# Kernel tuning notes

Hardware: AMD Instinct MI355X
Metric: run time of the kernel (lower is better)

Reference implementation:

```python
import jax, jax.numpy as jnp
import numpy as np

B, C, H, W = 2, 128, 64, 64
CR4 = C // 4  # hidden width of linear_weight / bias branches
SOFTMAX_SCALE = 1.0


def _leaky(z):
    return jnp.where(z >= 0, z, 0.2 * z)


def _conv1x1(x, w, b):
    # x: [B,Ci,H,W], w: [Co,Ci], b: [Co]
    return jnp.einsum('oc,bchw->bohw', w, x) + b[None, :, None, None]


def setup_inputs() -> dict:
    key = jax.random.key(0)
    ks = jax.random.split(key, 16)
    def n(k, shape, s=0.05):
        return jax.random.normal(k, shape, jnp.float32) * s
    return {
        'x': jax.random.normal(ks[0], (B, C, H, W), jnp.float32),
        'value_w': n(ks[1], (C, C)), 'value_b': n(ks[2], (C,)),
        'query_w': n(ks[3], (C, C)), 'query_b': n(ks[4], (C,)),
        'lw1_w': n(ks[5], (CR4, C)), 'lw1_b': n(ks[6], (CR4,)),
        'lw2_w': n(ks[7], (1, CR4)), 'lw2_b': n(ks[8], (1,)),
        'bi1_w': n(ks[9], (CR4, C)), 'bi1_b': n(ks[10], (CR4,)),
        'bi2_w': n(ks[11], (1, CR4)), 'bi2_b': n(ks[12], (1,)),
        'lin_w': n(ks[13], (C, C, 3, 3)), 'lin_b': n(ks[14], (C,)),
    }


def reference(x, value_w, value_b, query_w, query_b,
              lw1_w, lw1_b, lw2_w, lw2_b,
              bi1_w, bi1_b, bi2_w, bi2_b,
              lin_w, lin_b):
    # value / query 1x1 projections
    x1 = _conv1x1(x, value_w, value_b)   # [B,C,H,W]
    x2 = _conv1x1(x, query_w, query_b)   # [B,C,H,W]
    # dynamic per-pixel weight / bias maps (two 1x1 convs + LeakyReLU)
    wei = _conv1x1(_leaky(_conv1x1(x2, lw1_w, lw1_b)), lw2_w, lw2_b)  # [B,1,H,W]
    bii = _conv1x1(_leaky(_conv1x1(x2, bi1_w, bi1_b)), bi2_w, bi2_b)  # [B,1,H,W]

    Bn, Cn, Hn, Wn = x.shape
    L = Hn * Wn  # one 1x1 patch per spatial location (ksize=1, stride=1)
    # query patches [B,L,C]; normalize each patch to (at least 1e-4) unit norm
    wq = x2.transpose(0, 2, 3, 1).reshape(Bn, L, Cn)
    wnorm = wq / jnp.maximum(jnp.linalg.norm(wq, axis=2, keepdims=True), 1e-4)
    # attention scores: per-sample conv2d(xi, wi_normed) == batched matmul
    yi = jnp.einsum('bchw,blc->blhw', x2, wnorm)  # [B,L,H,W]
    # sparse gating
    sparse = jax.nn.relu(yi - yi.mean(axis=1, keepdims=True) * wei + bii)
    sr = (sparse != 0.0).astype(yi.dtype)
    yi = yi * sparse
    yi = jax.nn.softmax(yi * SOFTMAX_SCALE, axis=1)
    yi = jnp.maximum(yi * sr, 1e-8)
    # reconstruct with value patches (conv_transpose2d with 1x1 kernels)
    raw = x1.transpose(0, 2, 3, 1).reshape(Bn, L, Cn)
    out = jnp.einsum('blhw,blc->bchw', yi, raw)  # / (ksize*ksize) == /1
    # final 3x3 conv + LeakyReLU + residual
    y = jax.lax.conv_general_dilated(out, lin_w, (1, 1), 'SAME',
                                     dimension_numbers=('NCHW', 'OIHW', 'NCHW'))
    y = _leaky(y + lin_b[None, :, None, None])
    return y + x
```

## Files before the change

### kernel.cpp

```cpp
#include <hip/hip_runtime.h>
#include <hip/hip_bf16.h>
#include <math.h>

#define BB 2
#define C 128
#define L 4096
#define CR4 32
#define RS 4

typedef unsigned short ushort_t;
typedef __attribute__((ext_vector_type(8))) short s16x8;
typedef __attribute__((ext_vector_type(4))) float f32x4;

__device__ inline float leaky(float z) { return (z >= 0.f) ? z : 0.2f * z; }

__device__ inline unsigned short f2bf(float f) {
    unsigned int u = __builtin_bit_cast(unsigned int, f);
    unsigned int r = (u + 0x7fffu + ((u >> 16) & 1u)) >> 16;
    return (unsigned short)r;
}
__device__ inline float bf2f(unsigned short b) {
    unsigned int u = ((unsigned int)b) << 16;
    return __builtin_bit_cast(float, u);
}
__device__ inline unsigned int cvtpk(float lo, float hi) {
    unsigned int r;
    asm("v_cvt_pk_bf16_f32 %0, %1, %2" : "=v"(r) : "v"(lo), "v"(hi));
    return r;
}

__global__ __launch_bounds__(256) void k_wcomp(
    const float* __restrict__ vw, const float* __restrict__ vb,
    const float* __restrict__ qw, const float* __restrict__ qb,
    const float* __restrict__ lw1w, const float* __restrict__ lw1b,
    const float* __restrict__ bi1w, const float* __restrict__ bi1b,
    ushort_t* __restrict__ WQV, float* __restrict__ biasv)
{
    const int mt = blockIdx.x;
    const int t = threadIdx.x;
    const int kk = t >> 6, lane = t & 63;
    const int row = mt * 16 + (lane & 15);
    const int k0 = kk * 32 + (lane >> 4) * 8;
    s16x8 v;
    if (row < 128) {
        #pragma unroll
        for (int j = 0; j < 8; ++j) v[j] = (short)f2bf(vw[row * 128 + k0 + j]);
    } else if (row < 256) {
        #pragma unroll
        for (int j = 0; j < 8; ++j) v[j] = (short)f2bf(qw[(row - 128) * 128 + k0 + j]);
    } else {
        const float* w1 = (row < 288) ? lw1w + (row - 256) * 128
                                      : bi1w + (row - 288) * 128;
        float acc[8] = {0.f, 0.f, 0.f, 0.f, 0.f, 0.f, 0.f, 0.f};
        #pragma unroll 2
        for (int k = 0; k < 128; ++k) {
            float wv_ = w1[k];
            const float* qr = qw + k * 128 + k0;
            #pragma unroll
            for (int j = 0; j < 8; ++j) acc[j] = fmaf(wv_, qr[j], acc[j]);
        }
        #pragma unroll
        for (int j = 0; j < 8; ++j) v[j] = (short)f2bf(acc[j]);
    }
    *(s16x8*)(WQV + ((size_t)(mt * 4 + kk) * 64 + lane) * 8) = v;

    if (t < 16) {
        int rr = mt * 16 + t;
        float bv;
        if (rr < 128) bv = vb[rr];
        else if (rr < 256) bv = qb[rr - 128];
        else {
            const float* w1 = (rr < 288) ? lw1w + (rr - 256) * 128
                                         : bi1w + (rr - 288) * 128;
            float a = (rr < 288) ? lw1b[rr - 256] : bi1b[rr - 288];
            for (int k = 0; k < 128; ++k) a = fmaf(w1[k], qb[k], a);
            bv = a;
        }
        biasv[rr] = bv;
    }
}

__global__ __launch_bounds__(256, 1) void k_proj2(
    const float* __restrict__ x, const ushort_t* __restrict__ WQV,
    const float* __restrict__ biasv,
    const float* __restrict__ lw2w, const float* __restrict__ lw2b,
    const float* __restrict__ bi2w, const float* __restrict__ bi2b,
    ushort_t* __restrict__ x2a, ushort_t* __restrict__ x1g,
    float* __restrict__ weiA, float* __restrict__ biiA, float* __restrict__ scA,
    float* __restrict__ cpart)
{
    __shared__ __align__(16) char smem[16384 + 1536];
    char* xT = smem;
    float* biasLDS = (float*)(smem + 16384);
    float* w2LDS = biasLDS + 320;

    const int t = threadIdx.x;
    const int blk = blockIdx.x;
    const int part = blockIdx.y;
    const int b = blk >> 6;
    const int p0 = (blk & 63) * 64;
    const int wv = t >> 6, lane = t & 63, n = lane & 15, g = lane >> 4;

    biasLDS[t] = biasv[t];
    if (t < 64) {
        biasLDS[256 + t] = biasv[256 + t];
        w2LDS[t] = (t < 32) ? lw2w[t] : bi2w[t - 32];
    }

    const int pl = t & 63, cg = t >> 6;
    const float* xb = x + (size_t)b * C * L + p0 + pl;
    #pragma unroll
    for (int i = 0; i < 16; ++i) {
        int c = cg * 32 + i * 2;
        float v0 = xb[(size_t)c * L];
        float v1 = xb[(size_t)(c + 1) * L];
        int slot = c >> 3;
        int offs = (c * 2) & 15;
        int byte = pl * 256 + (((slot ^ (pl & 15)) << 4) | offs);
        *(unsigned int*)(xT + byte) = cvtpk(v0, v1);
    }
    __syncthreads();

    const int brow = wv * 16 + n;
    const int p = p0 + wv * 16 + n;
    const size_t bL = (size_t)b * L;

    if (part == 0) {
        const int mtm[12] = {0, 1, 2, 3, 4, 5, 6, 7, 16, 17, 18, 19};
        f32x4 acc[12];
        #pragma unroll
        for (int i = 0; i < 12; ++i) acc[i] = (f32x4){0.f, 0.f, 0.f, 0.f};
        #pragma unroll
        for (int kk = 0; kk < 4; ++kk) {
            const s16x8 bfr = *(const s16x8*)(xT + brow * 256 + (((4 * kk + g) ^ n) << 4));
            #pragma unroll
            for (int i = 0; i < 12; ++i) {
                const s16x8 afr = *(const s16x8*)(WQV + ((size_t)(mtm[i] * 4 + kk) * 64 + lane) * 8);
                acc[i] = __builtin_amdgcn_mfma_f32_16x16x32_bf16(afr, bfr, acc[i], 0, 0, 0);
            }
        }
        #pragma unroll
        for (int i = 0; i < 12; ++i) {
            const f32x4 bv = *(const f32x4*)(biasLDS + mtm[i] * 16 + g * 4);
            acc[i][0] += bv[0]; acc[i][1] += bv[1];
            acc[i][2] += bv[2]; acc[i][3] += bv[3];
        }
        #pragma unroll
        for (int i = 0; i < 8; ++i)
            #pragma unroll
            for (int r = 0; r < 4; ++r)
                x1g[((size_t)b * C + i * 16 + g * 4 + r) * L + p] = f2bf(acc[i][r]);
        float pw = 0.f, pbb = 0.f;
        #pragma unroll
        for (int i = 8; i < 10; ++i)
            #pragma unroll
            for (int r = 0; r < 4; ++r)
                pw = fmaf(w2LDS[(i - 8) * 16 + g * 4 + r], leaky(acc[i][r]), pw);
        #pragma unroll
        for (int i = 10; i < 12; ++i)
            #pragma unroll
            for (int r = 0; r < 4; ++r)
                pbb = fmaf(w2LDS[32 + (i - 10) * 16 + g * 4 + r], leaky(acc[i][r]), pbb);
        pw += __shfl_xor(pw, 16, 64);  pw += __shfl_xor(pw, 32, 64);
        pbb += __shfl_xor(pbb, 16, 64); pbb += __shfl_xor(pbb, 32, 64);
        if (g == 0) {
            weiA[bL + p] = pw + lw2b[0];
            biiA[bL + p] = pbb + bi2b[0];
        }
    } else {
        f32x4 acc[8];
        #pragma unroll
        for (int i = 0; i < 8; ++i) acc[i] = (f32x4){0.f, 0.f, 0.f, 0.f};
        #pragma unroll
        for (int kk = 0; kk < 4; ++kk) {
            const s16x8 bfr = *(const s16x8*)(xT + brow * 256 + (((4 * kk + g) ^ n) << 4));
            #pragma unroll
            for (int i = 0; i < 8; ++i) {
                const s16x8 afr = *(const s16x8*)(WQV + ((size_t)((8 + i) * 4 + kk) * 64 + lane) * 8);
                acc[i] = __builtin_amdgcn_mfma_f32_16x16x32_bf16(afr, bfr, acc[i], 0, 0, 0);
            }
        }
        #pragma unroll
        for (int i = 0; i < 8; ++i) {
            const f32x4 bv = *(const f32x4*)(biasLDS + (8 + i) * 16 + g * 4);
            acc[i][0] += bv[0]; acc[i][1] += bv[1];
            acc[i][2] += bv[2]; acc[i][3] += bv[3];
        }
        float pn = 0.f;
        #pragma unroll
        for (int i = 0; i < 8; ++i)
            #pragma unroll
            for (int r = 0; r < 4; ++r) pn = fmaf(acc[i][r], acc[i][r], pn);
        pn += __shfl_xor(pn, 16, 64);
        pn += __shfl_xor(pn, 32, 64);
        float scv = fmaxf(sqrtf(pn), 1e-4f);
        float dinv = 1.f / scv;
        if (g == 0) scA[bL + p] = scv;
        #pragma unroll
        for (int i = 0; i < 8; ++i) {
            uint2 uu;
            uu.x = cvtpk(acc[i][0] * dinv, acc[i][1] * dinv);
            uu.y = cvtpk(acc[i][2] * dinv, acc[i][3] * dinv);
            *(uint2*)(x2a + (bL + p) * C + i * 16 + g * 4) = uu;
        }
        float sv[32];
        #pragma unroll
        for (int i = 0; i < 8; ++i)
            #pragma unroll
            for (int r = 0; r < 4; ++r)
                sv[i * 4 + r] = acc[i][r] * dinv;
        #pragma unroll
        for (int mask = 1; mask <= 8; mask <<= 1)
            #pragma unroll
            for (int i = 0; i < 32; ++i)
                sv[i] += __shfl_xor(sv[i], mask, 64);
        __syncthreads();
        float* sumsh = (float*)xT;
        if (n == 0) {
            #pragma unroll
            for (int i = 0; i < 32; ++i) {
                int ch = (i >> 2) * 16 + g * 4 + (i & 3);
                sumsh[wv * 128 + ch] = sv[i];
            }
        }
        __syncthreads();
        if (t < 128)
            cpart[(size_t)blk * 128 + t] =
                (sumsh[t] + sumsh[128 + t]) + (sumsh[256 + t] + sumsh[384 + t]);
    }
}

__global__ __launch_bounds__(128) void k_cb(
    const float* __restrict__ cpart, float* __restrict__ cbv)
{
    const int b = blockIdx.x, t = threadIdx.x;
    float s = 0.f;
    #pragma unroll 4
    for (int j = 0; j < 64; ++j) s += cpart[(size_t)(b * 64 + j) * 128 + t];
    cbv[b * 128 + t] = s * (1.f / (float)L);
}

__global__ __launch_bounds__(256, 2) void k_attn(
    const ushort_t* __restrict__ x2a, const ushort_t* __restrict__ x1g,
    const float* __restrict__ scA, const float* __restrict__ weiA,
    const float* __restrict__ biiA, const float* __restrict__ cbv,
    ushort_t* __restrict__ Opb, float* __restrict__ Mp, float* __restrict__ Zp)
{
    __shared__ __align__(16) char smem[73728];

    const int t = threadIdx.x;
    const int w = t >> 6, lane = t & 63, n = lane & 15, g = lane >> 4;
    char* Pw = smem + 65536 + w * 2048;

    const int blk = blockIdx.x;
    const int q = blk & (RS - 1);
    const int colt = (blk >> 2) & 63;
    const int b = blk >> 8;
    const int p = colt * 64 + w * 16 + n;
    const size_t bL = (size_t)b * L;

    const s16x8* qrow = (const s16x8*)(x2a + (bL + p) * C);
    const float scp = scA[bL + p];
    s16x8 bq[4];
    float dot = 0.f;
    #pragma unroll
    for (int kk = 0; kk < 4; ++kk) {
        s16x8 raw = qrow[kk * 4 + g];
        const float* cbp = cbv + b * 128 + kk * 32 + g * 8;
        s16x8 u;
        #pragma unroll
        for (int j = 0; j < 8; ++j) {
            float rv = bf2f((unsigned short)raw[j]) * scp;
            u[j] = (short)f2bf(rv);
            dot = fmaf(cbp[j], rv, dot);
        }
        bq[kk] = u;
    }
    dot += __shfl_xor(dot, 16, 64);
    dot += __shfl_xor(dot, 32, 64);
    const float tq = fmaf(weiA[bL + p], dot, -biiA[bL + p]);

    f32x4 Oacc[8];
    #pragma unroll
    for (int ct = 0; ct < 8; ++ct) Oacc[ct] = (f32x4){0.f, 0.f, 0.f, 0.f};
    float Mrun = 0.f, Zrun = 0.f;

    const int l0base = q * (L / RS);
    const char* x2src = (const char*)(x2a + (bL + l0base) * C);
    const char* x1src = (const char*)(x1g + (size_t)b * C * L);

    #define STAGE_X2(buf, tile_)                                                         \
        {   const char* sb = x2src + (size_t)(tile_) * 64 * 256;                          \
            _Pragma("unroll")                                                             \
            for (int rr = 0; rr < 4; ++rr) {                                              \
                int slot = rr * 256 + t;                                                  \
                int lrow = slot >> 4, uu = slot & 15;                                     \
                const char* gp = sb + lrow * 256 + (((uu ^ (lrow & 7))) << 4);            \
                char* lp = (buf) + ((rr * 256 + w * 64) << 4);                            \
                __builtin_amdgcn_global_load_lds(                                         \
                    (const __attribute__((address_space(1))) unsigned int*)gp,            \
                    (__attribute__((address_space(3))) unsigned int*)lp, 16, 0, 0);       \
            } }
    #define STAGE_X1(buf, l0_)                                                            \
        {   _Pragma("unroll")                                                             \
            for (int rr = 0; rr < 4; ++rr) {                                              \
                int slot = rr * 256 + t;                                                  \
                int cr = slot >> 3, uu = slot & 7;                                        \
                const char* gp = x1src + ((size_t)cr * L + (l0_) + ((uu ^ (cr & 7)) << 3)) * 2; \
                char* lp = (buf) + ((rr * 256 + w * 64) << 4);                            \
                __builtin_amdgcn_global_load_lds(                                         \
                    (const __attribute__((address_space(1))) unsigned int*)gp,            \
                    (__attribute__((address_space(3))) unsigned int*)lp, 16, 0, 0);       \
            } }

    char* Abuf0 = smem;          char* Abuf1 = smem + 16384;
    char* Xbuf0 = smem + 32768;  char* Xbuf1 = smem + 49152;

    STAGE_X2(Abuf0, 0);
    STAGE_X1(Xbuf0, l0base);
    __syncthreads();

    const int swz = n & 7;
    const int NT = L / RS / 64;

    #pragma unroll 1
    for (int tile = 0; tile < NT; ++tile) {
        char* Ab = (tile & 1) ? Abuf1 : Abuf0;
        char* Xb = (tile & 1) ? Xbuf1 : Xbuf0;
        if (tile + 1 < NT) {
            char* An = (tile & 1) ? Abuf0 : Abuf1;
            char* Xn = (tile & 1) ? Xbuf0 : Xbuf1;
            STAGE_X2(An, tile + 1);
            STAGE_X1(Xn, l0base + (tile + 1) * 64);
        }

        f32x4 s4[4];
        #pragma unroll
        for (int lt = 0; lt < 4; ++lt) s4[lt] = (f32x4){0.f, 0.f, 0.f, 0.f};
        __builtin_amdgcn_s_setprio(1);
        #pragma unroll
        for (int kk = 0; kk < 4; ++kk) {
            #pragma unroll
            for (int lt = 0; lt < 4; ++lt) {
                const s16x8 a = *(const s16x8*)(Ab + (16 * lt + n) * 256 +
                                                (((4 * kk + g) ^ swz) << 4));
                s4[lt] = __builtin_amdgcn_mfma_f32_16x16x32_bf16(a, bq[kk], s4[lt], 0, 0, 0);
            }
        }
        __builtin_amdgcn_s_setprio(0);

        float vv[16], sps[16];
        #pragma unroll
        for (int lt = 0; lt < 4; ++lt) {
            #pragma unroll
            for (int r = 0; r < 4; ++r) {
                float s = s4[lt][r];
                float sp = s - tq;
                sps[lt * 4 + r] = sp;
                vv[lt * 4 + r] = s * fmaxf(sp, 0.f);
            }
        }
        float tm[8];
        #pragma unroll
        for (int i = 0; i < 8; ++i) tm[i] = fmaxf(vv[2 * i], vv[2 * i + 1]);
        #pragma unroll
        for (int i = 0; i < 4; ++i) tm[i] = fmaxf(tm[2 * i], tm[2 * i + 1]);
        float tmax = fmaxf(fmaxf(tm[0], tm[1]), fmaxf(tm[2], tm[3]));
        tmax = fmaxf(tmax, __shfl_xor(tmax, 16, 64));
        tmax = fmaxf(tmax, __shfl_xor(tmax, 32, 64));

        if (!__all(tmax <= Mrun + 8.f)) {
            float Mn = fmaxf(Mrun, tmax);
            float so = __expf(Mrun - Mn);
            Mrun = Mn;
            Zrun *= so;
            #pragma unroll
            for (int ct = 0; ct < 8; ++ct) {
                Oacc[ct][0] *= so; Oacc[ct][1] *= so;
                Oacc[ct][2] *= so; Oacc[ct][3] *= so;
            }
        }

        #pragma unroll
        for (int lt = 0; lt < 4; ++lt) {
            float e0 = __expf(vv[lt * 4 + 0] - Mrun);
            float e1 = __expf(vv[lt * 4 + 1] - Mrun);
            float e2 = __expf(vv[lt * 4 + 2] - Mrun);
            float e3 = __expf(vv[lt * 4 + 3] - Mrun);
            Zrun += (e0 + e1) + (e2 + e3);
            float p0 = sps[lt * 4 + 0] > 0.f ? e0 : 0.f;
            float p1 = sps[lt * 4 + 1] > 0.f ? e1 : 0.f;
            float p2 = sps[lt * 4 + 2] > 0.f ? e2 : 0.f;
            float p3 = sps[lt * 4 + 3] > 0.f ? e3 : 0.f;
            int ulog = 2 * lt + (g >> 1);
            int byte = n * 128 + ((ulog ^ swz) << 4) + ((g & 1) << 3);
            uint2 uu;
            uu.x = cvtpk(p0, p1);
            uu.y = cvtpk(p2, p3);
            *(uint2*)(Pw + byte) = uu;
        }

        __builtin_amdgcn_s_setprio(1);
        #pragma unroll
        for (int kk2 = 0; kk2 < 2; ++kk2) {
            const s16x8 pb = *(const s16x8*)(Pw + n * 128 + (((4 * kk2 + g) ^ swz) << 4));
            #pragma unroll
            for (int ct = 0; ct < 8; ++ct) {
                const s16x8 a = *(const s16x8*)(Xb + (16 * ct + n) * 128 +
                                                (((4 * kk2 + g) ^ swz) << 4));
                Oacc[ct] = __builtin_amdgcn_mfma_f32_16x16x32_bf16(a, pb, Oacc[ct], 0, 0, 0);
            }
        }
        __builtin_amdgcn_s_setprio(0);
        __syncthreads();
    }
    #undef STAGE_X2
    #undef STAGE_X1

    float z = Zrun;
    z += __shfl_xor(z, 16, 64);
    z += __shfl_xor(z, 32, 64);

    const size_t sset = (size_t)(q * BB + b);
    ushort_t* ob = Opb + (sset * L + p) * C;
    #pragma unroll
    for (int ct = 0; ct < 8; ++ct) {
        uint2 uu;
        uu.x = cvtpk(Oacc[ct][0], Oacc[ct][1]);
        uu.y = cvtpk(Oacc[ct][2], Oacc[ct][3]);
        *(uint2*)(ob + 16 * ct + 4 * g) = uu;
    }
    if (g == 0) {
        Mp[sset * L + p] = Mrun;
        Zp[sset * L + p] = z;
    }
}

__global__ __launch_bounds__(256) void k_merge(
    const ushort_t* __restrict__ Opb, const float* __restrict__ Mp,
    const float* __restrict__ Zp, ushort_t* __restrict__ attnb)
{
    const int idx = blockIdx.x * 256 + threadIdx.x;
    const int c4 = idx & 31;
    const int p = (idx >> 5) & 4095;
    const int b = idx >> 17;
    size_t is[RS];
    float M = -1e30f;
    float Mq[RS], Zq[RS];
    #pragma unroll
    for (int q = 0; q < RS; ++q) {
        is[q] = (size_t)(q * BB + b) * L + p;
        Mq[q] = Mp[is[q]];
        Zq[q] = Zp[is[q]];
        M = fmaxf(M, Mq[q]);
    }
    float Zt = 0.f;
    float aq[RS];
    #pragma unroll
    for (int q = 0; q < RS; ++q) {
        aq[q] = __expf(Mq[q] - M);
        Zt = fmaf(Zq[q], aq[q], Zt);
    }
    float zi = 1.f / Zt;
    float r0 = 0.f, r1 = 0.f, r2 = 0.f, r3 = 0.f;
    #pragma unroll
    for (int q = 0; q < RS; ++q) {
        float s = aq[q] * zi;
        const ushort4 o = *(const ushort4*)(Opb + is[q] * C + c4 * 4);
        r0 = fmaf(bf2f(o.x), s, r0);
        r1 = fmaf(bf2f(o.y), s, r1);
        r2 = fmaf(bf2f(o.z), s, r2);
        r3 = fmaf(bf2f(o.w), s, r3);
    }
    uint2 uu;
    uu.x = cvtpk(r0, r1);
    uu.y = cvtpk(r2, r3);
    *(uint2*)(attnb + ((size_t)b * L + p) * C + c4 * 4) = uu;
}

__global__ __launch_bounds__(256) void k_wrep(
    const float* __restrict__ lw, ushort_t* __restrict__ W3)
{
    const int tid = blockIdx.x * 256 + threadIdx.x;
    const int s = tid >> 9;
    const int r = tid & 511;
    const int mt = r >> 6, lane = r & 63;
    const int co = mt * 16 + (lane & 15), g = lane >> 4;
    const int kk = s >> 2, kc = s & 3;
    const int ci0 = kc * 32 + g * 8;
    s16x8 v;
    #pragma unroll
    for (int j = 0; j < 8; ++j)
        v[j] = (short)f2bf(lw[((size_t)co * 128 + ci0 + j) * 9 + kk]);
    *(s16x8*)(W3 + (size_t)tid * 8) = v;
}

__global__ __launch_bounds__(256, 1) void k_conv(
    const ushort_t* __restrict__ attnb, const float* __restrict__ x,
    const ushort_t* __restrict__ W3, const float* __restrict__ lb,
    float* __restrict__ out)
{
    __shared__ __align__(16) char smem[65536];
    char* attnT = smem;
    char* Wb0 = smem + 49152;
    char* Wb1 = smem + 57344;

    const int t = threadIdx.x;
    const int wv = t >> 6, lane = t & 63, n = lane & 15, g = lane >> 4;
    const int h = blockIdx.x;
    const int half = blockIdx.y;
    const int b = blockIdx.z;

    const char* asrc = (const char*)attnb + ((size_t)b * L + (size_t)(h - 1) * 64) * C * 2;
    #pragma unroll
    for (int rr = 0; rr < 3; ++rr) {
        if ((unsigned)(h - 1 + rr) < 64u) {
            #pragma unroll
            for (int qq = 0; qq < 4; ++qq) {
                int slot = rr * 1024 + qq * 256 + t;
                int lrow = slot >> 4, uu = slot & 15;
                const char* gp = asrc + lrow * 256 + ((uu ^ (lrow & 7)) << 4);
                char* lp = attnT + ((rr * 1024 + qq * 256 + wv * 64) << 4);
                __builtin_amdgcn_global_load_lds(
                    (const __attribute__((address_space(1))) unsigned int*)gp,
                    (__attribute__((address_space(3))) unsigned int*)lp, 16, 0, 0);
            }
        }
    }
    #define STAGE_W(buf, s_)                                                              \
        {   _Pragma("unroll")                                                             \
            for (int qq = 0; qq < 2; ++qq) {                                              \
                const char* gp = (const char*)W3 + ((size_t)(s_) * 512 + qq * 256 + t) * 16; \
                char* lp = (buf) + ((qq * 256 + wv * 64) << 4);                           \
                __builtin_amdgcn_global_load_lds(                                         \
                    (const __attribute__((address_space(1))) unsigned int*)gp,            \
                    (__attribute__((address_space(3))) unsigned int*)lp, 16, 0, 0);       \
            } }

    STAGE_W(Wb0, 0);
    __syncthreads();

    f32x4 acc[2][2];
    #pragma unroll
    for (int mi = 0; mi < 2; ++mi)
        #pragma unroll
        for (int nt = 0; nt < 2; ++nt) acc[mi][nt] = (f32x4){0.f, 0.f, 0.f, 0.f};

    const s16x8 zer = {0, 0, 0, 0, 0, 0, 0, 0};

    #pragma unroll 1
    for (int s = 0; s < 36; ++s) {
        char* Wc = (s & 1) ? Wb1 : Wb0;
        if (s + 1 < 36) {
            char* Wn = (s & 1) ? Wb0 : Wb1;
            STAGE_W(Wn, s + 1);
        }
        const int kk = s >> 2, kc = s & 3;
        const int kh = kk / 3, kw = kk - kh * 3;
        const int dh = kh - 1, dw = kw - 1;
        const bool hval = ((unsigned)(h + dh) < 64u);

        s16x8 af0 = *(const s16x8*)(Wc + (((2 * wv) * 64 + lane) << 4));
        s16x8 af1 = *(const s16x8*)(Wc + (((2 * wv + 1) * 64 + lane) << 4));

        #pragma unroll
        for (int nt = 0; nt < 2; ++nt) {
            int pl = half * 32 + nt * 16 + n;
            int wd = pl + dw;
            bool val = hval && ((unsigned)wd < 64u);
            int wc = wd < 0 ? 0 : (wd > 63 ? 63 : wd);
            int lrow = (dh + 1) * 64 + wc;
            s16x8 bf_ = *(const s16x8*)(attnT + lrow * 256 +
                                        (((kc * 4 + g) ^ (lrow & 7)) << 4));
            if (!val) bf_ = zer;
            acc[0][nt] = __builtin_amdgcn_mfma_f32_16x16x32_bf16(af0, bf_, acc[0][nt], 0, 0, 0);
            acc[1][nt] = __builtin_amdgcn_mfma_f32_16x16x32_bf16(af1, bf_, acc[1][nt], 0, 0, 0);
        }
        __syncthreads();
    }
    #undef STAGE_W

    const float* xb = x + (size_t)b * C * L + h * 64;
    float* ob = out + (size_t)b * C * L + h * 64;
    #pragma unroll
    for (int mi = 0; mi < 2; ++mi) {
        #pragma unroll
        for (int r = 0; r < 4; ++r) {
            int co = (2 * wv + mi) * 16 + g * 4 + r;
            float bias = lb[co];
            #pragma unroll
            for (int nt = 0; nt < 2; ++nt) {
                int p_ = half * 32 + nt * 16 + n;
                float v = leaky(acc[mi][nt][r] + bias);
                ob[(size_t)co * L + p_] = v + xb[(size_t)co * L + p_];
            }
        }
    }
}

extern "C" void kernel_launch(void* const* d_in, const int* in_sizes, int n_in,
                              void* d_out, int out_size, void* d_ws, size_t ws_size,
                              hipStream_t stream) {
    const float* x     = (const float*)d_in[0];
    const float* vw    = (const float*)d_in[1];
    const float* vb    = (const float*)d_in[2];
    const float* qw    = (const float*)d_in[3];
    const float* qb    = (const float*)d_in[4];
    const float* lw1w  = (const float*)d_in[5];
    const float* lw1b  = (const float*)d_in[6];
    const float* lw2w  = (const float*)d_in[7];
    const float* lw2b  = (const float*)d_in[8];
    const float* bi1w  = (const float*)d_in[9];
    const float* bi1b  = (const float*)d_in[10];
    const float* bi2w  = (const float*)d_in[11];
    const float* bi2b  = (const float*)d_in[12];
    const float* lw    = (const float*)d_in[13];
    const float* lb    = (const float*)d_in[14];
    float* out = (float*)d_out;

    char* ws = (char*)d_ws;
    ushort_t* x2a  = (ushort_t*)ws;
    ushort_t* x1g  = (ushort_t*)(ws + 2097152);
    ushort_t* Opb  = (ushort_t*)(ws + 4194304);
    ushort_t* WQV  = (ushort_t*)(ws + 4194304);
    float* biasv = (float*)(ws + 4194304 + 81920);
    float* weiA  = (float*)(ws + 12582912);
    float* biiA  = weiA + BB * L;
    float* scA   = biiA + BB * L;
    float* Mp    = scA + BB * L;
    float* Zp    = Mp + RS * BB * L;
    float* cpart = Zp + RS * BB * L;
    float* cbv   = cpart + 128 * 128;
    ushort_t* W3 = x1g;
    ushort_t* attnb = x2a;

    hipLaunchKernelGGL(k_wcomp, dim3(20), dim3(256), 0, stream,
                       vw, vb, qw, qb, lw1w, lw1b, bi1w, bi1b, WQV, biasv);

    hipLaunchKernelGGL(k_proj2, dim3(128, 2), dim3(256), 0, stream,
                       x, WQV, biasv, lw2w, lw2b, bi2w, bi2b,
                       x2a, x1g, weiA, biiA, scA, cpart);

    hipLaunchKernelGGL(k_cb, dim3(BB), dim3(128), 0, stream, cpart, cbv);

    hipLaunchKernelGGL(k_attn, dim3(BB * 64 * RS), dim3(256), 0, stream,
                       x2a, x1g, scA, weiA, biiA, cbv, Opb, Mp, Zp);

    hipLaunchKernelGGL(k_wrep, dim3(72), dim3(256), 0, stream, lw, W3);

    hipLaunchKernelGGL(k_merge, dim3(BB * L * C / 4 / 256), dim3(256), 0, stream,
                       Opb, Mp, Zp, attnb);

    hipLaunchKernelGGL(k_conv, dim3(64, 2, BB), dim3(256), 0, stream,
                       attnb, x, W3, lb, out);
}
```

Before: 105.4 us.

## Fold small kernels into neighbours and stream conv weights from global

The channel-mean reduction kernel is removed: each attention block now sums cpart itself into shared memory, with the query preparation moved after the first barrier. The merge and weight-repack kernels are combined into one launch that branches on block index. The 3x3 conv stops staging weights through LDS with a barrier per step and instead prefetches weight fragments straight from global into registers two steps ahead. Together these remove two launches and the per-step conv syncs, at the cost of redundant cpart reads in every attention block and global-latency exposure on the conv weight loads.

```diff
diff --git a/kernel.cpp b/kernel.cpp
--- a/kernel.cpp
+++ b/kernel.cpp
@@ -230,23 +230,14 @@
     }
 }
 
-__global__ __launch_bounds__(128) void k_cb(
-    const float* __restrict__ cpart, float* __restrict__ cbv)
-{
-    const int b = blockIdx.x, t = threadIdx.x;
-    float s = 0.f;
-    #pragma unroll 4
-    for (int j = 0; j < 64; ++j) s += cpart[(size_t)(b * 64 + j) * 128 + t];
-    cbv[b * 128 + t] = s * (1.f / (float)L);
-}
-
 __global__ __launch_bounds__(256, 2) void k_attn(
     const ushort_t* __restrict__ x2a, const ushort_t* __restrict__ x1g,
     const float* __restrict__ scA, const float* __restrict__ weiA,
-    const float* __restrict__ biiA, const float* __restrict__ cbv,
+    const float* __restrict__ biiA, const float* __restrict__ cpart,
     ushort_t* __restrict__ Opb, float* __restrict__ Mp, float* __restrict__ Zp)
 {
     __shared__ __align__(16) char smem[73728];
+    __shared__ float cbsh[128];
 
     const int t = threadIdx.x;
     const int w = t >> 6, lane = t & 63, n = lane & 15, g = lane >> 4;
@@ -259,31 +250,13 @@
     const int p = colt * 64 + w * 16 + n;
     const size_t bL = (size_t)b * L;
 
-    const s16x8* qrow = (const s16x8*)(x2a + (bL + p) * C);
-    const float scp = scA[bL + p];
-    s16x8 bq[4];
-    float dot = 0.f;
-    #pragma unroll
-    for (int kk = 0; kk < 4; ++kk) {
-        s16x8 raw = qrow[kk * 4 + g];
-        const float* cbp = cbv + b * 128 + kk * 32 + g * 8;
-        s16x8 u;
-        #pragma unroll
-        for (int j = 0; j < 8; ++j) {
-            float rv = bf2f((unsigned short)raw[j]) * scp;
-            u[j] = (short)f2bf(rv);
-            dot = fmaf(cbp[j], rv, dot);
-        }
-        bq[kk] = u;
-    }
-    dot += __shfl_xor(dot, 16, 64);
-    dot += __shfl_xor(dot, 32, 64);
-    const float tq = fmaf(weiA[bL + p], dot, -biiA[bL + p]);
-
-    f32x4 Oacc[8];
-    #pragma unroll
-    for (int ct = 0; ct < 8; ++ct) Oacc[ct] = (f32x4){0.f, 0.f, 0.f, 0.f};
-    float Mrun = 0.f, Zrun = 0.f;
+    if (t < 128) {
+        float s = 0.f;
+        const float* cp = cpart + (size_t)(b * 64) * 128 + t;
+        #pragma unroll 4
+        for (int j = 0; j < 64; ++j) s += cp[(size_t)j * 128];
+        cbsh[t] = s * (1.f / (float)L);
+    }
 
     const int l0base = q * (L / RS);
     const char* x2src = (const char*)(x2a + (bL + l0base) * C);
@@ -320,6 +293,32 @@
     STAGE_X1(Xbuf0, l0base);
     __syncthreads();
 
+    const s16x8* qrow = (const s16x8*)(x2a + (bL + p) * C);
+    const float scp = scA[bL + p];
+    s16x8 bq[4];
+    float dot = 0.f;
+    #pragma unroll
+    for (int kk = 0; kk < 4; ++kk) {
+        s16x8 raw = qrow[kk * 4 + g];
+        const float* cbp = cbsh + kk * 32 + g * 8;
+        s16x8 u;
+        #pragma unroll
+        for (int j = 0; j < 8; ++j) {
+            float rv = bf2f((unsigned short)raw[j]) * scp;
+            u[j] = (short)f2bf(rv);
+            dot = fmaf(cbp[j], rv, dot);
+        }
+        bq[kk] = u;
+    }
+    dot += __shfl_xor(dot, 16, 64);
+    dot += __shfl_xor(dot, 32, 64);
+    const float tq = fmaf(weiA[bL + p], dot, -biiA[bL + p]);
+
+    f32x4 Oacc[8];
+    #pragma unroll
+    for (int ct = 0; ct < 8; ++ct) Oacc[ct] = (f32x4){0.f, 0.f, 0.f, 0.f};
+    float Mrun = 0.f, Zrun = 0.f;
+
     const int swz = n & 7;
     const int NT = L / RS / 64;
 
@@ -436,63 +435,64 @@
     }
 }
 
-__global__ __launch_bounds__(256) void k_merge(
+__global__ __launch_bounds__(256) void k_mergewrep(
     const ushort_t* __restrict__ Opb, const float* __restrict__ Mp,
-    const float* __restrict__ Zp, ushort_t* __restrict__ attnb)
-{
-    const int idx = blockIdx.x * 256 + threadIdx.x;
-    const int c4 = idx & 31;
-    const int p = (idx >> 5) & 4095;
-    const int b = idx >> 17;
-    size_t is[RS];
-    float M = -1e30f;
-    float Mq[RS], Zq[RS];
-    #pragma unroll
-    for (int q = 0; q < RS; ++q) {
-        is[q] = (size_t)(q * BB + b) * L + p;
-        Mq[q] = Mp[is[q]];
-        Zq[q] = Zp[is[q]];
-        M = fmaxf(M, Mq[q]);
-    }
-    float Zt = 0.f;
-    float aq[RS];
-    #pragma unroll
-    for (int q = 0; q < RS; ++q) {
-        aq[q] = __expf(Mq[q] - M);
-        Zt = fmaf(Zq[q], aq[q], Zt);
-    }
-    float zi = 1.f / Zt;
-    float r0 = 0.f, r1 = 0.f, r2 = 0.f, r3 = 0.f;
-    #pragma unroll
-    for (int q = 0; q < RS; ++q) {
-        float s = aq[q] * zi;
-        const ushort4 o = *(const ushort4*)(Opb + is[q] * C + c4 * 4);
-        r0 = fmaf(bf2f(o.x), s, r0);
-        r1 = fmaf(bf2f(o.y), s, r1);
-        r2 = fmaf(bf2f(o.z), s, r2);
-        r3 = fmaf(bf2f(o.w), s, r3);
-    }
-    uint2 uu;
-    uu.x = cvtpk(r0, r1);
-    uu.y = cvtpk(r2, r3);
-    *(uint2*)(attnb + ((size_t)b * L + p) * C + c4 * 4) = uu;
-}
-
-__global__ __launch_bounds__(256) void k_wrep(
+    const float* __restrict__ Zp, ushort_t* __restrict__ attnb,
     const float* __restrict__ lw, ushort_t* __restrict__ W3)
 {
-    const int tid = blockIdx.x * 256 + threadIdx.x;
-    const int s = tid >> 9;
-    const int r = tid & 511;
-    const int mt = r >> 6, lane = r & 63;
-    const int co = mt * 16 + (lane & 15), g = lane >> 4;
-    const int kk = s >> 2, kc = s & 3;
-    const int ci0 = kc * 32 + g * 8;
-    s16x8 v;
-    #pragma unroll
-    for (int j = 0; j < 8; ++j)
-        v[j] = (short)f2bf(lw[((size_t)co * 128 + ci0 + j) * 9 + kk]);
-    *(s16x8*)(W3 + (size_t)tid * 8) = v;
+    const int blkid = blockIdx.x;
+    const int t = threadIdx.x;
+    if (blkid < 1024) {
+        const int idx = blkid * 256 + t;
+        const int c4 = idx & 31;
+        const int p = (idx >> 5) & 4095;
+        const int b = idx >> 17;
+        size_t is[RS];
+        float M = -1e30f;
+        float Mq[RS], Zq[RS];
+        #pragma unroll
+        for (int q = 0; q < RS; ++q) {
+            is[q] = (size_t)(q * BB + b) * L + p;
+            Mq[q] = Mp[is[q]];
+            Zq[q] = Zp[is[q]];
+            M = fmaxf(M, Mq[q]);
+        }
+        float Zt = 0.f;
+        float aq[RS];
+        #pragma unroll
+        for (int q = 0; q < RS; ++q) {
+            aq[q] = __expf(Mq[q] - M);
+            Zt = fmaf(Zq[q], aq[q], Zt);
+        }
+        float zi = 1.f / Zt;
+        float r0 = 0.f, r1 = 0.f, r2 = 0.f, r3 = 0.f;
+        #pragma unroll
+        for (int q = 0; q < RS; ++q) {
+            float s = aq[q] * zi;
+            const ushort4 o = *(const ushort4*)(Opb + is[q] * C + c4 * 4);
+            r0 = fmaf(bf2f(o.x), s, r0);
+            r1 = fmaf(bf2f(o.y), s, r1);
+            r2 = fmaf(bf2f(o.z), s, r2);
+            r3 = fmaf(bf2f(o.w), s, r3);
+        }
+        uint2 uu;
+        uu.x = cvtpk(r0, r1);
+        uu.y = cvtpk(r2, r3);
+        *(uint2*)(attnb + ((size_t)b * L + p) * C + c4 * 4) = uu;
+    } else {
+        const int tid = (blkid - 1024) * 256 + t;
+        const int s = tid >> 9;
+        const int r = tid & 511;
+        const int mt = r >> 6, lane = r & 63;
+        const int co = mt * 16 + (lane & 15), g = lane >> 4;
+        const int kk = s >> 2, kc = s & 3;
+        const int ci0 = kc * 32 + g * 8;
+        s16x8 v;
+        #pragma unroll
+        for (int j = 0; j < 8; ++j)
+            v[j] = (short)f2bf(lw[((size_t)co * 128 + ci0 + j) * 9 + kk]);
+        *(s16x8*)(W3 + (size_t)tid * 8) = v;
+    }
 }
 
 __global__ __launch_bounds__(256, 1) void k_conv(
@@ -500,10 +500,7 @@
     const ushort_t* __restrict__ W3, const float* __restrict__ lb,
     float* __restrict__ out)
 {
-    __shared__ __align__(16) char smem[65536];
-    char* attnT = smem;
-    char* Wb0 = smem + 49152;
-    char* Wb1 = smem + 57344;
+    __shared__ __align__(16) char attnT[49152];
 
     const int t = threadIdx.x;
     const int wv = t >> 6, lane = t & 63, n = lane & 15, g = lane >> 4;
@@ -527,17 +524,12 @@
             }
         }
     }
-    #define STAGE_W(buf, s_)                                                              \
-        {   _Pragma("unroll")                                                             \
-            for (int qq = 0; qq < 2; ++qq) {                                              \
-                const char* gp = (const char*)W3 + ((size_t)(s_) * 512 + qq * 256 + t) * 16; \
-                char* lp = (buf) + ((qq * 256 + wv * 64) << 4);                           \
-                __builtin_amdgcn_global_load_lds(                                         \
-                    (const __attribute__((address_space(1))) unsigned int*)gp,            \
-                    (__attribute__((address_space(3))) unsigned int*)lp, 16, 0, 0);       \
-            } }
-
-    STAGE_W(Wb0, 0);
+
+    #define WROW(s_, mi_) (*(const s16x8*)(W3 + (((size_t)(s_) * 8 + 2 * wv + (mi_)) * 64 + lane) * 8))
+
+    s16x8 w0a = WROW(0, 0), w0b = WROW(0, 1);
+    s16x8 w1a = WROW(1, 0), w1b = WROW(1, 1);
+
     __syncthreads();
 
     f32x4 acc[2][2];
@@ -548,37 +540,37 @@
 
     const s16x8 zer = {0, 0, 0, 0, 0, 0, 0, 0};
 
+    #define CONV_STEP(s_, af0_, af1_)                                                    \
+    {   const int kk = (s_) >> 2, kc = (s_) & 3;                                         \
+        const int kh = kk / 3, kw = kk - kh * 3;                                         \
+        const int dh = kh - 1, dw = kw - 1;                                              \
+        const bool hval = ((unsigned)(h + dh) < 64u);                                    \
+        _Pragma("unroll")                                                                \
+        for (int nt = 0; nt < 2; ++nt) {                                                 \
+            int pl = half * 32 + nt * 16 + n;                                            \
+            int wd = pl + dw;                                                            \
+            bool val = hval && ((unsigned)wd < 64u);                                     \
+            int wc = wd < 0 ? 0 : (wd > 63 ? 63 : wd);                                   \
+            int lrow = (dh + 1) * 64 + wc;                                               \
+            s16x8 bf_ = *(const s16x8*)(attnT + lrow * 256 +                             \
+                                        (((kc * 4 + g) ^ (lrow & 7)) << 4));             \
+            if (!val) bf_ = zer;                                                         \
+            acc[0][nt] = __builtin_amdgcn_mfma_f32_16x16x32_bf16(af0_, bf_, acc[0][nt], 0, 0, 0); \
+            acc[1][nt] = __builtin_amdgcn_mfma_f32_16x16x32_bf16(af1_, bf_, acc[1][nt], 0, 0, 0); \
+        }                                                                                \
+    }
+
     #pragma unroll 1
-    for (int s = 0; s < 36; ++s) {
-        char* Wc = (s & 1) ? Wb1 : Wb0;
-        if (s + 1 < 36) {
-            char* Wn = (s & 1) ? Wb0 : Wb1;
-            STAGE_W(Wn, s + 1);
-        }
-        const int kk = s >> 2, kc = s & 3;
-        const int kh = kk / 3, kw = kk - kh * 3;
-        const int dh = kh - 1, dw = kw - 1;
-        const bool hval = ((unsigned)(h + dh) < 64u);
-
-        s16x8 af0 = *(const s16x8*)(Wc + (((2 * wv) * 64 + lane) << 4));
-        s16x8 af1 = *(const s16x8*)(Wc + (((2 * wv + 1) * 64 + lane) << 4));
-
-        #pragma unroll
-        for (int nt = 0; nt < 2; ++nt) {
-            int pl = half * 32 + nt * 16 + n;
-            int wd = pl + dw;
-            bool val = hval && ((unsigned)wd < 64u);
-            int wc = wd < 0 ? 0 : (wd > 63 ? 63 : wd);
-            int lrow = (dh + 1) * 64 + wc;
-            s16x8 bf_ = *(const s16x8*)(attnT + lrow * 256 +
-                                        (((kc * 4 + g) ^ (lrow & 7)) << 4));
-            if (!val) bf_ = zer;
-            acc[0][nt] = __builtin_amdgcn_mfma_f32_16x16x32_bf16(af0, bf_, acc[0][nt], 0, 0, 0);
-            acc[1][nt] = __builtin_amdgcn_mfma_f32_16x16x32_bf16(af1, bf_, acc[1][nt], 0, 0, 0);
-        }
-        __syncthreads();
-    }
-    #undef STAGE_W
+    for (int s = 0; s < 36; s += 2) {
+        s16x8 af0 = w0a, af1 = w0b;
+        if (s + 2 < 36) { w0a = WROW(s + 2, 0); w0b = WROW(s + 2, 1); }
+        CONV_STEP(s, af0, af1)
+        af0 = w1a; af1 = w1b;
+        if (s + 3 < 36) { w1a = WROW(s + 3, 0); w1b = WROW(s + 3, 1); }
+        CONV_STEP(s + 1, af0, af1)
+    }
+    #undef CONV_STEP
+    #undef WROW
 
     const float* xb = x + (size_t)b * C * L + h * 64;
     float* ob = out + (size_t)b * C * L + h * 64;
@@ -630,7 +622,6 @@
     float* Mp    = scA + BB * L;
     float* Zp    = Mp + RS * BB * L;
     float* cpart = Zp + RS * BB * L;
-    float* cbv   = cpart + 128 * 128;
     ushort_t* W3 = x1g;
     ushort_t* attnb = x2a;
 
@@ -641,15 +632,11 @@
                        x, WQV, biasv, lw2w, lw2b, bi2w, bi2b,
                        x2a, x1g, weiA, biiA, scA, cpart);
 
-    hipLaunchKernelGGL(k_cb, dim3(BB), dim3(128), 0, stream, cpart, cbv);
-
     hipLaunchKernelGGL(k_attn, dim3(BB * 64 * RS), dim3(256), 0, stream,
-                       x2a, x1g, scA, weiA, biiA, cbv, Opb, Mp, Zp);
-
-    hipLaunchKernelGGL(k_wrep, dim3(72), dim3(256), 0, stream, lw, W3);
-
-    hipLaunchKernelGGL(k_merge, dim3(BB * L * C / 4 / 256), dim3(256), 0, stream,
-                       Opb, Mp, Zp, attnb);
+                       x2a, x1g, scA, weiA, biiA, cpart, Opb, Mp, Zp);
+
+    hipLaunchKernelGGL(k_mergewrep, dim3(1096), dim3(256), 0, stream,
+                       Opb, Mp, Zp, attnb, lw, W3);
 
     hipLaunchKernelGGL(k_conv, dim3(64, 2, BB), dim3(256), 0, stream,
                        attnb, x, W3, lb, out);
```

Result: faster. 99.51 us (-5.6%).
